# Optimization experiments

Measured on AMD Instinct MI355X. Metric: run time of the kernel, lower is better.

## Reference

```python
import jax, jax.numpy as jnp
import numpy as np

N = 100000
E = 1600000
B = 64
EPS = 1e-5


def setup_inputs() -> dict:
    key = jax.random.key(0)
    ks = jax.random.split(key, 20)
    x = jax.random.normal(ks[0], (N, 3), dtype=jnp.float32)
    edge_index = jax.random.randint(ks[1], (2, E), 0, N, dtype=jnp.int64)
    batch = jnp.sort(jax.random.randint(ks[2], (N,), 0, B, dtype=jnp.int64))

    def lin(k, fan_in, fan_out):
        s = 1.0 / np.sqrt(fan_in)
        kw, kb = jax.random.split(k)
        W = jax.random.uniform(kw, (fan_in, fan_out), minval=-s, maxval=s, dtype=jnp.float32)
        b = jax.random.uniform(kb, (fan_out,), minval=-s, maxval=s, dtype=jnp.float32)
        return W, b

    W1, b1 = lin(ks[3], 3, 16)
    W2, b2 = lin(ks[4], 16, 32)
    W3, b3 = lin(ks[5], 32, 64)
    fcW, fcb = lin(ks[6], 64, 10)
    g1 = jnp.ones((16,), jnp.float32); be1 = jnp.zeros((16,), jnp.float32)
    g2 = jnp.ones((32,), jnp.float32); be2 = jnp.zeros((32,), jnp.float32)
    g3 = jnp.ones((64,), jnp.float32); be3 = jnp.zeros((64,), jnp.float32)
    return {"x": x, "edge_index": edge_index, "batch": batch,
            "W1": W1, "b1": b1, "g1": g1, "be1": be1,
            "W2": W2, "b2": b2, "g2": g2, "be2": be2,
            "W3": W3, "b3": b3, "g3": g3, "be3": be3,
            "fcW": fcW, "fcb": fcb}


def _gcn_conv(x, W, b, row, col, deg_inv_sqrt):
    # PyG GCNConv: add self-loops (pre-appended in row/col), symmetric norm,
    # scatter-add aggregation at target nodes, then bias.
    xw = x @ W                                   # [N, d_out]
    norm = deg_inv_sqrt[row] * deg_inv_sqrt[col]  # [E+N]
    msg = xw[row] * norm[:, None]                 # gather + scale
    out = jax.ops.segment_sum(msg, col, num_segments=N)
    return out + b


def _bn_relu(x, gamma, beta):
    mean = jnp.mean(x, axis=0)
    var = jnp.mean(jnp.square(x - mean), axis=0)  # biased var (torch BN)
    xh = (x - mean) * jax.lax.rsqrt(var + EPS)
    return jax.nn.relu(xh * gamma + beta)


def reference(x, edge_index, batch, W1, b1, g1, be1, W2, b2, g2, be2,
              W3, b3, g3, be3, fcW, fcb):
    loops = jnp.arange(N, dtype=edge_index.dtype)
    row = jnp.concatenate([edge_index[0], loops])
    col = jnp.concatenate([edge_index[1], loops])
    deg = jax.ops.segment_sum(jnp.ones_like(col, dtype=x.dtype), col, num_segments=N)
    dis = jax.lax.rsqrt(deg)  # deg >= 1 due to self-loops

    h = _bn_relu(_gcn_conv(x, W1, b1, row, col, dis), g1, be1)
    h = _bn_relu(_gcn_conv(h, W2, b2, row, col, dis), g2, be2)
    h = _bn_relu(_gcn_conv(h, W3, b3, row, col, dis), g3, be3)

    sums = jax.ops.segment_sum(h, batch, num_segments=B)          # [B, 64]
    cnts = jax.ops.segment_sum(jnp.ones((N,), h.dtype), batch, num_segments=B)
    pooled = sums / jnp.maximum(cnts, 1.0)[:, None]
    return pooled @ fcW + fcb                                     # [B, 10]
```

## Files before the change

### kernel.cpp

```cpp
#include <hip/hip_runtime.h>

#define N_NODES 100000
#define N_EDGES 1600000
#define B_GRAPHS 64
#define BN_EPS 1e-5
#define NBMAX 3200

#define NBUCK 256
#define BUCK_NODES 392
#define PART_CHUNK 4096
#define NB_PART 391

#define QSCALE 2048.0f
#define QINV   4.8828125e-4f

typedef _Float16 half4_t __attribute__((ext_vector_type(4)));
typedef short short4_t __attribute__((ext_vector_type(4)));
typedef int intv2 __attribute__((ext_vector_type(2)));
typedef int intv4 __attribute__((ext_vector_type(4)));
typedef float floatv4 __attribute__((ext_vector_type(4)));

static inline int cdiv(long long a, int b) { return (int)((a + b - 1) / b); }

__device__ __forceinline__ short q16(float v) {
    int q = __float2int_rn(v * QSCALE);
    q = q > 32767 ? 32767 : (q < -32768 ? -32768 : q);
    return (short)q;
}

__global__ void part_hist_kernel(const int* __restrict__ col, int* __restrict__ bucket_cnt) {
    __shared__ int h[NBUCK];
    for (int i = threadIdx.x; i < NBUCK; i += 256) h[i] = 0;
    __syncthreads();
    long long ebase = (long long)blockIdx.x * PART_CHUNK;
    int n = (N_EDGES - ebase < PART_CHUNK) ? (int)(N_EDGES - ebase) : PART_CHUNK;
    for (int i = threadIdx.x; i < n; i += 256)
        atomicAdd(&h[col[ebase + i] / BUCK_NODES], 1);
    __syncthreads();
    for (int i = threadIdx.x; i < NBUCK; i += 256)
        if (h[i]) atomicAdd(&bucket_cnt[i], h[i]);
}

__global__ void part_scan_kernel(const int* __restrict__ bucket_cnt, int* __restrict__ bucket_base,
                                 int* __restrict__ bucket_cur) {
    __shared__ int s[NBUCK];
    int t = threadIdx.x;
    int v = bucket_cnt[t];
    s[t] = v;
    __syncthreads();
    for (int off = 1; off < NBUCK; off <<= 1) {
        int u = (t >= off) ? s[t - off] : 0;
        __syncthreads();
        s[t] += u;
        __syncthreads();
    }
    bucket_base[t] = s[t] - v;
    bucket_cur[t] = s[t] - v;
}

__global__ void part_scatter_kernel(const int* __restrict__ row, const int* __restrict__ col,
                                    int* __restrict__ bucket_cur, unsigned* __restrict__ part_edges) {
    __shared__ int h[NBUCK];
    __shared__ int base_s[NBUCK];
    __shared__ int cur_s[NBUCK];
    long long ebase = (long long)blockIdx.x * PART_CHUNK;
    int n = (N_EDGES - ebase < PART_CHUNK) ? (int)(N_EDGES - ebase) : PART_CHUNK;
    for (int i = threadIdx.x; i < NBUCK; i += 256) h[i] = 0;
    __syncthreads();
    for (int i = threadIdx.x; i < n; i += 256)
        atomicAdd(&h[col[ebase + i] / BUCK_NODES], 1);
    __syncthreads();
    for (int i = threadIdx.x; i < NBUCK; i += 256) {
        int c = h[i];
        base_s[i] = c ? atomicAdd(&bucket_cur[i], c) : 0;
        cur_s[i] = 0;
    }
    __syncthreads();
    for (int i = threadIdx.x; i < n; i += 256) {
        int r = row[ebase + i], c = col[ebase + i];
        int bkt = c / BUCK_NODES;
        int p = base_s[bkt] + atomicAdd(&cur_s[bkt], 1);
        part_edges[p] = ((unsigned)r << 9) | (unsigned)(c - bkt * BUCK_NODES);
    }
}

__global__ void csr_build_kernel(const int* __restrict__ bucket_base, const unsigned* __restrict__ part_edges,
                                 int* __restrict__ row_ptr, int* __restrict__ deg,
                                 float* __restrict__ dis, int* __restrict__ sorted_row,
                                 const float* __restrict__ x, short* __restrict__ xs4) {
    __shared__ int hist[BUCK_NODES];
    __shared__ int tsum[256];
    int b = blockIdx.x;
    int t = threadIdx.x;
    int nbase = b * BUCK_NODES;
    int ebase = bucket_base[b];
    int eend = (b == NBUCK - 1) ? N_EDGES : bucket_base[b + 1];
    int ne = eend - ebase;
    for (int i = t; i < BUCK_NODES; i += 256) hist[i] = 0;
    __syncthreads();
    for (int i = t; i < ne; i += 256)
        atomicAdd(&hist[part_edges[ebase + i] & 511u], 1);
    __syncthreads();
    int a0 = 0, a1 = 0;
    if (t < BUCK_NODES / 2) { a0 = hist[2 * t]; a1 = hist[2 * t + 1]; tsum[t] = a0 + a1; }
    else tsum[t] = 0;
    __syncthreads();
    for (int off = 1; off < 256; off <<= 1) {
        int u = (t >= off) ? tsum[t - off] : 0;
        __syncthreads();
        tsum[t] += u;
        __syncthreads();
    }
    if (t < BUCK_NODES / 2) {
        int excl = tsum[t] - (a0 + a1);
        hist[2 * t] = excl;
        hist[2 * t + 1] = excl + a0;
        int n0 = nbase + 2 * t, n1 = n0 + 1;
        if (n0 < N_NODES) {
            row_ptr[n0] = ebase + excl;
            deg[n0] = a0;
            dis[n0] = rsqrtf((float)a0 + 1.0f);
        }
        if (n1 < N_NODES) {
            row_ptr[n1] = ebase + excl + a0;
            deg[n1] = a1;
            dis[n1] = rsqrtf((float)a1 + 1.0f);
        }
    }
    __syncthreads();
    for (int i = t; i < ne; i += 256) {
        unsigned e = part_edges[ebase + i];
        int p = atomicAdd(&hist[e & 511u], 1);
        sorted_row[ebase + p] = (int)(e >> 9);
    }
    for (int i = t; i < BUCK_NODES; i += 256) {
        int n = nbase + i;
        if (n < N_NODES) {
            float d = dis[n];
            short4_t v;
            v.x = q16(x[n * 3 + 0] * d);
            v.y = q16(x[n * 3 + 1] * d);
            v.z = q16(x[n * 3 + 2] * d);
            v.w = 0;
            ((short4_t*)xs4)[n] = v;
        }
    }
}

template <int WPL> struct VecSel;
template <> struct VecSel<2> { using type = intv2; };
template <> struct VecSel<4> { using type = intv4; };

template <int IN, int OUT, int INSTRIDE, int WPL>
__global__ void gather_mm_kernel(const int* __restrict__ row_ptr, const int* __restrict__ deg,
                                 const int* __restrict__ sorted_row, const float* __restrict__ dis,
                                 const short* __restrict__ hs, const float* __restrict__ W,
                                 const float* __restrict__ b, _Float16* __restrict__ pre,
                                 double* __restrict__ part_s, double* __restrict__ part_q) {
    using V = typename VecSel<WPL>::type;
    const int FPL = 2 * WPL;
    const int LPN = INSTRIDE / FPL;
    const int NPW = 64 / LPN;
    const int NPB = 4 * NPW;
    const int UNROLL = 8;
    __shared__ __align__(16) float lds_agg[NPB * INSTRIDE];
    __shared__ double s_s[256];
    __shared__ double s_q[256];
    int tid = threadIdx.x;
    int wv = tid >> 6, lane = tid & 63;
    int jn = wv * NPW + lane / LPN;
    int p = lane % LPN;
    int n = blockIdx.x * NPB + jn;
    if (n < N_NODES) {
        int start = row_ptr[n];
        int d = deg[n];
        const int* sr = sorted_row + start;
        const V* hv = (const V*)hs;
        V v = hv[n * LPN + p];
        int acc[FPL];
#pragma unroll
        for (int w = 0; w < WPL; w++) {
            acc[2 * w] = (int)(short)v[w];
            acc[2 * w + 1] = v[w] >> 16;
        }
        int j = 0;
        for (; j + UNROLL <= d; j += UNROLL) {
            V a[UNROLL];
#pragma unroll
            for (int u = 0; u < UNROLL; u++) a[u] = hv[sr[j + u] * LPN + p];
#pragma unroll
            for (int u = 0; u < UNROLL; u++) {
#pragma unroll
                for (int w = 0; w < WPL; w++) {
                    acc[2 * w] += (int)(short)a[u][w];
                    acc[2 * w + 1] += a[u][w] >> 16;
                }
            }
        }
        for (; j < d; j++) {
            V a = hv[sr[j] * LPN + p];
#pragma unroll
            for (int w = 0; w < WPL; w++) {
                acc[2 * w] += (int)(short)a[w];
                acc[2 * w + 1] += a[w] >> 16;
            }
        }
        float dn = dis[n] * QINV;
        float* dst = &lds_agg[(jn * LPN + p) * FPL];
#pragma unroll
        for (int k = 0; k < FPL; k++) dst[k] = dn * (float)acc[k];
    }
    __syncthreads();

    const int NG = 256 / OUT;
    int o = tid % OUT;
    int g = tid / OUT;
    float wreg[IN];
#pragma unroll
    for (int k = 0; k < IN; k++) wreg[k] = W[k * OUT + o];
    float bo = b[o];
    double my_s = 0.0, my_q = 0.0;
    for (int j2 = g; j2 < NPB; j2 += NG) {
        int nn = blockIdx.x * NPB + j2;
        if (nn < N_NODES) {
            float acc = bo;
            const floatv4* src = (const floatv4*)&lds_agg[j2 * INSTRIDE];
#pragma unroll
            for (int q = 0; q < INSTRIDE / 4; q++) {
                floatv4 vq = src[q];
#pragma unroll
                for (int c = 0; c < 4; c++) {
                    if (4 * q + c < IN) acc += vq[c] * wreg[4 * q + c];
                }
            }
            _Float16 hq = (_Float16)acc;
            pre[nn * OUT + o] = hq;
            float fq = (float)hq;
            my_s += (double)fq;
            my_q += (double)fq * (double)fq;
        }
    }
    s_s[tid] = my_s;
    s_q[tid] = my_q;
    __syncthreads();
    if (tid < OUT) {
        double ts = 0.0, tq = 0.0;
        for (int k = tid; k < 256; k += OUT) { ts += s_s[k]; tq += s_q[k]; }
        part_s[(long long)tid * NBMAX + blockIdx.x] = ts;
        part_q[(long long)tid * NBMAX + blockIdx.x] = tq;
    }
}

__global__ void bn_finalize_kernel(const double* __restrict__ part_s, const double* __restrict__ part_q,
                                   int nb, float* __restrict__ bn_mean, float* __restrict__ bn_rstd) {
    __shared__ double s_s[256];
    __shared__ double s_q[256];
    int o = blockIdx.x;
    int t = threadIdx.x;
    double ms = 0.0, mq = 0.0;
    for (int k = t; k < nb; k += 256) {
        ms += part_s[(long long)o * NBMAX + k];
        mq += part_q[(long long)o * NBMAX + k];
    }
    s_s[t] = ms;
    s_q[t] = mq;
    __syncthreads();
    for (int off = 128; off > 0; off >>= 1) {
        if (t < off) { s_s[t] += s_s[t + off]; s_q[t] += s_q[t + off]; }
        __syncthreads();
    }
    if (t == 0) {
        double mean = s_s[0] / (double)N_NODES;
        double var = s_q[0] / (double)N_NODES - mean * mean;
        bn_mean[o] = (float)mean;
        bn_rstd[o] = (float)(1.0 / sqrt(var + BN_EPS));
    }
}

template <int F>
__global__ void bn_relu_kernel(const _Float16* __restrict__ pre, const float* __restrict__ bn_mean,
                               const float* __restrict__ bn_rstd, const float* __restrict__ g,
                               const float* __restrict__ be, const float* __restrict__ dis,
                               short* __restrict__ out) {
    const int GP = F / 4;
    int t = blockIdx.x * blockDim.x + threadIdx.x;
    const int total = N_NODES * GP;
    if (t >= total) return;
    int gi = t % GP;
    int f0 = gi * 4;
    half4_t v = ((const half4_t*)pre)[t];
    float d = dis[t / GP];
    short4_t o;
#pragma unroll
    for (int k = 0; k < 4; k++) {
        int f = f0 + k;
        float y = ((float)v[k] - bn_mean[f]) * bn_rstd[f] * g[f] + be[f];
        y = y > 0.f ? y : 0.f;
        o[k] = q16(y * d);
    }
    ((short4_t*)out)[t] = o;
}

#define POOL_CHUNK 32
__global__ void pool_kernel(const _Float16* __restrict__ pre, const int* __restrict__ batch,
                            const float* __restrict__ bn_mean, const float* __restrict__ bn_rstd,
                            const float* __restrict__ g, const float* __restrict__ be,
                            float* __restrict__ pooled, float* __restrict__ cnt) {
    int wave = (blockIdx.x * blockDim.x + threadIdx.x) >> 6;
    int lane = threadIdx.x & 63;
    int start = wave * POOL_CHUNK;
    if (start >= N_NODES) return;
    int end = start + POOL_CHUNK;
    if (end > N_NODES) end = N_NODES;
    float A = bn_rstd[lane] * g[lane];
    float B = be[lane] - bn_mean[lane] * A;
    int cur = batch[start];
    float acc = 0.f;
    float c = 0.f;
    int i = start;
    for (; i + 4 <= end; i += 4) {
        int b0 = batch[i], b1 = batch[i + 1], b2 = batch[i + 2], b3 = batch[i + 3];
        float v0 = fmaxf(0.f, fmaf((float)pre[(long long)i * 64 + lane], A, B));
        float v1 = fmaxf(0.f, fmaf((float)pre[(long long)(i + 1) * 64 + lane], A, B));
        float v2 = fmaxf(0.f, fmaf((float)pre[(long long)(i + 2) * 64 + lane], A, B));
        float v3 = fmaxf(0.f, fmaf((float)pre[(long long)(i + 3) * 64 + lane], A, B));
        if (b0 != cur) { atomicAdd(&pooled[cur * 64 + lane], acc); if (lane == 0) atomicAdd(&cnt[cur], c); acc = 0.f; c = 0.f; cur = b0; }
        acc += v0; c += 1.f;
        if (b1 != cur) { atomicAdd(&pooled[cur * 64 + lane], acc); if (lane == 0) atomicAdd(&cnt[cur], c); acc = 0.f; c = 0.f; cur = b1; }
        acc += v1; c += 1.f;
        if (b2 != cur) { atomicAdd(&pooled[cur * 64 + lane], acc); if (lane == 0) atomicAdd(&cnt[cur], c); acc = 0.f; c = 0.f; cur = b2; }
        acc += v2; c += 1.f;
        if (b3 != cur) { atomicAdd(&pooled[cur * 64 + lane], acc); if (lane == 0) atomicAdd(&cnt[cur], c); acc = 0.f; c = 0.f; cur = b3; }
        acc += v3; c += 1.f;
    }
    for (; i < end; i++) {
        int b = batch[i];
        if (b != cur) { atomicAdd(&pooled[cur * 64 + lane], acc); if (lane == 0) atomicAdd(&cnt[cur], c); acc = 0.f; c = 0.f; cur = b; }
        acc += fmaxf(0.f, fmaf((float)pre[(long long)i * 64 + lane], A, B)); c += 1.f;
    }
    atomicAdd(&pooled[cur * 64 + lane], acc);
    if (lane == 0) atomicAdd(&cnt[cur], c);
}

__global__ void final_kernel(const float* __restrict__ pooled, const float* __restrict__ cnt,
                             const float* __restrict__ fcW, const float* __restrict__ fcb,
                             float* __restrict__ out) {
    int t = blockIdx.x * blockDim.x + threadIdx.x;
    if (t >= B_GRAPHS * 10) return;
    int b = t / 10, j = t % 10;
    float inv = 1.0f / fmaxf(cnt[b], 1.0f);
    float acc = fcb[j];
#pragma unroll
    for (int f = 0; f < 64; f++) acc += pooled[b * 64 + f] * inv * fcW[f * 10 + j];
    out[t] = acc;
}

extern "C" void kernel_launch(void* const* d_in, const int* in_sizes, int n_in,
                              void* d_out, int out_size, void* d_ws, size_t ws_size,
                              hipStream_t stream) {
    const float* x  = (const float*)d_in[0];
    const int* ei   = (const int*)d_in[1];
    const int* batch= (const int*)d_in[2];
    const float* W1 = (const float*)d_in[3];  const float* b1 = (const float*)d_in[4];
    const float* g1 = (const float*)d_in[5];  const float* be1= (const float*)d_in[6];
    const float* W2 = (const float*)d_in[7];  const float* b2 = (const float*)d_in[8];
    const float* g2 = (const float*)d_in[9];  const float* be2= (const float*)d_in[10];
    const float* W3 = (const float*)d_in[11]; const float* b3 = (const float*)d_in[12];
    const float* g3 = (const float*)d_in[13]; const float* be3= (const float*)d_in[14];
    const float* fcW= (const float*)d_in[15]; const float* fcb= (const float*)d_in[16];
    float* out = (float*)d_out;

    const int* row = ei;
    const int* col = ei + N_EDGES;

    char* wp = (char*)d_ws;
    int*   bucket_cnt = (int*)wp;                wp += NBUCK * 4;
    float* pooled     = (float*)wp;              wp += 64 * 64 * 4;
    float* cnt        = (float*)wp;              wp += 64 * 4;
    const size_t ZERO_BYTES = NBUCK * 4 + 64 * 64 * 4 + 64 * 4;
    float* dis        = (float*)wp;              wp += N_NODES * 4;
    int*   deg_i      = (int*)wp;                wp += N_NODES * 4;
    int*   row_ptr    = (int*)wp;                wp += N_NODES * 4;
    int*   bucket_base= (int*)wp;                wp += NBUCK * 4;
    int*   bucket_cur = (int*)wp;                wp += NBUCK * 4;
    int*   sorted_row = (int*)wp;                wp += (size_t)N_EDGES * 4;
    unsigned* part_edges = (unsigned*)wp;        wp += (size_t)N_EDGES * 4;
    double* part_s    = (double*)wp;             wp += (size_t)NBMAX * 64 * 8;
    double* part_q    = (double*)wp;             wp += (size_t)NBMAX * 64 * 8;
    float* bn_mean    = (float*)wp;              wp += 64 * 4;
    float* bn_rstd    = (float*)wp;              wp += 64 * 4;
    short* xs4q       = (short*)wp;              wp += (size_t)N_NODES * 4 * 2;
    _Float16* PRE     = (_Float16*)wp;           wp += (size_t)N_NODES * 64 * 2;
    short* Hq         = (short*)wp;              wp += (size_t)N_NODES * 32 * 2;

    const int BS = 256;

    hipMemsetAsync(bucket_cnt, 0, ZERO_BYTES, stream);

    part_hist_kernel<<<NB_PART, 256, 0, stream>>>(col, bucket_cnt);
    part_scan_kernel<<<1, NBUCK, 0, stream>>>(bucket_cnt, bucket_base, bucket_cur);
    part_scatter_kernel<<<NB_PART, 256, 0, stream>>>(row, col, bucket_cur, part_edges);
    csr_build_kernel<<<NBUCK, 256, 0, stream>>>(bucket_base, part_edges, row_ptr, deg_i, dis, sorted_row, x, xs4q);

    const int NB1 = cdiv(N_NODES, 256);
    gather_mm_kernel<3, 16, 4, 2><<<NB1, 256, 0, stream>>>(
        row_ptr, deg_i, sorted_row, dis, xs4q, W1, b1, PRE, part_s, part_q);
    bn_finalize_kernel<<<16, 256, 0, stream>>>(part_s, part_q, NB1, bn_mean, bn_rstd);
    bn_relu_kernel<16><<<cdiv((long long)N_NODES * 4, BS), BS, 0, stream>>>(
        PRE, bn_mean, bn_rstd, g1, be1, dis, Hq);

    const int NB2 = cdiv(N_NODES, 128);
    gather_mm_kernel<16, 32, 16, 4><<<NB2, 256, 0, stream>>>(
        row_ptr, deg_i, sorted_row, dis, Hq, W2, b2, PRE, part_s, part_q);
    bn_finalize_kernel<<<32, 256, 0, stream>>>(part_s, part_q, NB2, bn_mean, bn_rstd);
    bn_relu_kernel<32><<<cdiv((long long)N_NODES * 8, BS), BS, 0, stream>>>(
        PRE, bn_mean, bn_rstd, g2, be2, dis, Hq);

    const int NB3 = cdiv(N_NODES, 64);
    gather_mm_kernel<32, 64, 32, 4><<<NB3, 256, 0, stream>>>(
        row_ptr, deg_i, sorted_row, dis, Hq, W3, b3, PRE, part_s, part_q);
    bn_finalize_kernel<<<64, 256, 0, stream>>>(part_s, part_q, NB3, bn_mean, bn_rstd);

    pool_kernel<<<cdiv((long long)cdiv(N_NODES, POOL_CHUNK) * 64, BS), BS, 0, stream>>>(
        PRE, batch, bn_mean, bn_rstd, g3, be3, pooled, cnt);
    final_kernel<<<1, B_GRAPHS * 10, 0, stream>>>(pooled, cnt, fcW, fcb, out);
}
```

Baseline: 266.0 us.

## Fold scan, BN finalize and final FC into last-block-done tails of producer kernels

Removes the separate part_scan, bn_finalize (three times) and final_kernel launches. Each producer kernel now takes an atomic done counter, and the last block to finish runs the follow-up reduction after a threadfence. This cuts five kernel launches and their launch gaps. In exchange, every block pays for an extra fence and atomic, and each finalize reduction now runs serially in one block instead of one block per feature.

```diff
diff --git a/kernel.cpp b/kernel.cpp
--- a/kernel.cpp
+++ b/kernel.cpp
@@ -28,8 +28,11 @@
     return (short)q;
 }
 
-__global__ void part_hist_kernel(const int* __restrict__ col, int* __restrict__ bucket_cnt) {
+__global__ void part_hist_kernel(const int* __restrict__ col, int* __restrict__ bucket_cnt,
+                                 int* __restrict__ bucket_base, int* __restrict__ bucket_cur,
+                                 int* __restrict__ done_ctr) {
     __shared__ int h[NBUCK];
+    __shared__ int is_last;
     for (int i = threadIdx.x; i < NBUCK; i += 256) h[i] = 0;
     __syncthreads();
     long long ebase = (long long)blockIdx.x * PART_CHUNK;
@@ -39,23 +42,24 @@
     __syncthreads();
     for (int i = threadIdx.x; i < NBUCK; i += 256)
         if (h[i]) atomicAdd(&bucket_cnt[i], h[i]);
-}
-
-__global__ void part_scan_kernel(const int* __restrict__ bucket_cnt, int* __restrict__ bucket_base,
-                                 int* __restrict__ bucket_cur) {
-    __shared__ int s[NBUCK];
+    __threadfence();
+    __syncthreads();
+    if (threadIdx.x == 0) is_last = (atomicAdd(done_ctr, 1) == gridDim.x - 1);
+    __syncthreads();
+    if (!is_last) return;
+    __threadfence();
     int t = threadIdx.x;
     int v = bucket_cnt[t];
-    s[t] = v;
+    h[t] = v;
     __syncthreads();
     for (int off = 1; off < NBUCK; off <<= 1) {
-        int u = (t >= off) ? s[t - off] : 0;
+        int u = (t >= off) ? h[t - off] : 0;
         __syncthreads();
-        s[t] += u;
+        h[t] += u;
         __syncthreads();
     }
-    bucket_base[t] = s[t] - v;
-    bucket_cur[t] = s[t] - v;
+    bucket_base[t] = h[t] - v;
+    bucket_cur[t] = h[t] - v;
 }
 
 __global__ void part_scatter_kernel(const int* __restrict__ row, const int* __restrict__ col,
@@ -156,7 +160,9 @@
                                  const int* __restrict__ sorted_row, const float* __restrict__ dis,
                                  const short* __restrict__ hs, const float* __restrict__ W,
                                  const float* __restrict__ b, _Float16* __restrict__ pre,
-                                 double* __restrict__ part_s, double* __restrict__ part_q) {
+                                 double* __restrict__ part_s, double* __restrict__ part_q,
+                                 int* __restrict__ done_ctr, float* __restrict__ bn_mean,
+                                 float* __restrict__ bn_rstd) {
     using V = typename VecSel<WPL>::type;
     const int FPL = 2 * WPL;
     const int LPN = INSTRIDE / FPL;
@@ -166,6 +172,7 @@
     __shared__ __align__(16) float lds_agg[NPB * INSTRIDE];
     __shared__ double s_s[256];
     __shared__ double s_q[256];
+    __shared__ int is_last;
     int tid = threadIdx.x;
     int wv = tid >> 6, lane = tid & 63;
     int jn = wv * NPW + lane / LPN;
@@ -249,31 +256,36 @@
         part_s[(long long)tid * NBMAX + blockIdx.x] = ts;
         part_q[(long long)tid * NBMAX + blockIdx.x] = tq;
     }
-}
-
-__global__ void bn_finalize_kernel(const double* __restrict__ part_s, const double* __restrict__ part_q,
-                                   int nb, float* __restrict__ bn_mean, float* __restrict__ bn_rstd) {
-    __shared__ double s_s[256];
-    __shared__ double s_q[256];
-    int o = blockIdx.x;
-    int t = threadIdx.x;
-    double ms = 0.0, mq = 0.0;
-    for (int k = t; k < nb; k += 256) {
-        ms += part_s[(long long)o * NBMAX + k];
-        mq += part_q[(long long)o * NBMAX + k];
-    }
-    s_s[t] = ms;
-    s_q[t] = mq;
-    __syncthreads();
-    for (int off = 128; off > 0; off >>= 1) {
-        if (t < off) { s_s[t] += s_s[t + off]; s_q[t] += s_q[t + off]; }
+
+    __threadfence();
+    __syncthreads();
+    if (tid == 0) is_last = (atomicAdd(done_ctr, 1) == gridDim.x - 1);
+    __syncthreads();
+    if (!is_last) return;
+    __threadfence();
+    {
+        const int TPF = 256 / OUT;
+        int fo = tid % OUT;
+        int fq = tid / OUT;
+        int nb = gridDim.x;
+        double ms = 0.0, mq = 0.0;
+        for (int k = fq; k < nb; k += TPF) {
+            ms += part_s[(long long)fo * NBMAX + k];
+            mq += part_q[(long long)fo * NBMAX + k];
+        }
+        s_s[tid] = ms;
+        s_q[tid] = mq;
         __syncthreads();
-    }
-    if (t == 0) {
-        double mean = s_s[0] / (double)N_NODES;
-        double var = s_q[0] / (double)N_NODES - mean * mean;
-        bn_mean[o] = (float)mean;
-        bn_rstd[o] = (float)(1.0 / sqrt(var + BN_EPS));
+        for (int off = TPF / 2; off > 0; off >>= 1) {
+            if (fq < off) { s_s[tid] += s_s[tid + off * OUT]; s_q[tid] += s_q[tid + off * OUT]; }
+            __syncthreads();
+        }
+        if (fq == 0) {
+            double mean = s_s[tid] / (double)N_NODES;
+            double var = s_q[tid] / (double)N_NODES - mean * mean;
+            bn_mean[fo] = (float)mean;
+            bn_rstd[fo] = (float)(1.0 / sqrt(var + BN_EPS));
+        }
     }
 }
 
@@ -305,54 +317,59 @@
 __global__ void pool_kernel(const _Float16* __restrict__ pre, const int* __restrict__ batch,
                             const float* __restrict__ bn_mean, const float* __restrict__ bn_rstd,
                             const float* __restrict__ g, const float* __restrict__ be,
-                            float* __restrict__ pooled, float* __restrict__ cnt) {
+                            float* __restrict__ pooled, float* __restrict__ cnt,
+                            int* __restrict__ done_ctr, const float* __restrict__ fcW,
+                            const float* __restrict__ fcb, float* __restrict__ out) {
+    __shared__ int is_last;
     int wave = (blockIdx.x * blockDim.x + threadIdx.x) >> 6;
     int lane = threadIdx.x & 63;
     int start = wave * POOL_CHUNK;
-    if (start >= N_NODES) return;
-    int end = start + POOL_CHUNK;
-    if (end > N_NODES) end = N_NODES;
-    float A = bn_rstd[lane] * g[lane];
-    float B = be[lane] - bn_mean[lane] * A;
-    int cur = batch[start];
-    float acc = 0.f;
-    float c = 0.f;
-    int i = start;
-    for (; i + 4 <= end; i += 4) {
-        int b0 = batch[i], b1 = batch[i + 1], b2 = batch[i + 2], b3 = batch[i + 3];
-        float v0 = fmaxf(0.f, fmaf((float)pre[(long long)i * 64 + lane], A, B));
-        float v1 = fmaxf(0.f, fmaf((float)pre[(long long)(i + 1) * 64 + lane], A, B));
-        float v2 = fmaxf(0.f, fmaf((float)pre[(long long)(i + 2) * 64 + lane], A, B));
-        float v3 = fmaxf(0.f, fmaf((float)pre[(long long)(i + 3) * 64 + lane], A, B));
-        if (b0 != cur) { atomicAdd(&pooled[cur * 64 + lane], acc); if (lane == 0) atomicAdd(&cnt[cur], c); acc = 0.f; c = 0.f; cur = b0; }
-        acc += v0; c += 1.f;
-        if (b1 != cur) { atomicAdd(&pooled[cur * 64 + lane], acc); if (lane == 0) atomicAdd(&cnt[cur], c); acc = 0.f; c = 0.f; cur = b1; }
-        acc += v1; c += 1.f;
-        if (b2 != cur) { atomicAdd(&pooled[cur * 64 + lane], acc); if (lane == 0) atomicAdd(&cnt[cur], c); acc = 0.f; c = 0.f; cur = b2; }
-        acc += v2; c += 1.f;
-        if (b3 != cur) { atomicAdd(&pooled[cur * 64 + lane], acc); if (lane == 0) atomicAdd(&cnt[cur], c); acc = 0.f; c = 0.f; cur = b3; }
-        acc += v3; c += 1.f;
-    }
-    for (; i < end; i++) {
-        int b = batch[i];
-        if (b != cur) { atomicAdd(&pooled[cur * 64 + lane], acc); if (lane == 0) atomicAdd(&cnt[cur], c); acc = 0.f; c = 0.f; cur = b; }
-        acc += fmaxf(0.f, fmaf((float)pre[(long long)i * 64 + lane], A, B)); c += 1.f;
-    }
-    atomicAdd(&pooled[cur * 64 + lane], acc);
-    if (lane == 0) atomicAdd(&cnt[cur], c);
-}
-
-__global__ void final_kernel(const float* __restrict__ pooled, const float* __restrict__ cnt,
-                             const float* __restrict__ fcW, const float* __restrict__ fcb,
-                             float* __restrict__ out) {
-    int t = blockIdx.x * blockDim.x + threadIdx.x;
-    if (t >= B_GRAPHS * 10) return;
-    int b = t / 10, j = t % 10;
-    float inv = 1.0f / fmaxf(cnt[b], 1.0f);
-    float acc = fcb[j];
-#pragma unroll
-    for (int f = 0; f < 64; f++) acc += pooled[b * 64 + f] * inv * fcW[f * 10 + j];
-    out[t] = acc;
+    if (start < N_NODES) {
+        int end = start + POOL_CHUNK;
+        if (end > N_NODES) end = N_NODES;
+        float A = bn_rstd[lane] * g[lane];
+        float B = be[lane] - bn_mean[lane] * A;
+        int cur = batch[start];
+        float acc = 0.f;
+        float c = 0.f;
+        int i = start;
+        for (; i + 4 <= end; i += 4) {
+            int b0 = batch[i], b1 = batch[i + 1], b2 = batch[i + 2], b3 = batch[i + 3];
+            float v0 = fmaxf(0.f, fmaf((float)pre[(long long)i * 64 + lane], A, B));
+            float v1 = fmaxf(0.f, fmaf((float)pre[(long long)(i + 1) * 64 + lane], A, B));
+            float v2 = fmaxf(0.f, fmaf((float)pre[(long long)(i + 2) * 64 + lane], A, B));
+            float v3 = fmaxf(0.f, fmaf((float)pre[(long long)(i + 3) * 64 + lane], A, B));
+            if (b0 != cur) { atomicAdd(&pooled[cur * 64 + lane], acc); if (lane == 0) atomicAdd(&cnt[cur], c); acc = 0.f; c = 0.f; cur = b0; }
+            acc += v0; c += 1.f;
+            if (b1 != cur) { atomicAdd(&pooled[cur * 64 + lane], acc); if (lane == 0) atomicAdd(&cnt[cur], c); acc = 0.f; c = 0.f; cur = b1; }
+            acc += v1; c += 1.f;
+            if (b2 != cur) { atomicAdd(&pooled[cur * 64 + lane], acc); if (lane == 0) atomicAdd(&cnt[cur], c); acc = 0.f; c = 0.f; cur = b2; }
+            acc += v2; c += 1.f;
+            if (b3 != cur) { atomicAdd(&pooled[cur * 64 + lane], acc); if (lane == 0) atomicAdd(&cnt[cur], c); acc = 0.f; c = 0.f; cur = b3; }
+            acc += v3; c += 1.f;
+        }
+        for (; i < end; i++) {
+            int b = batch[i];
+            if (b != cur) { atomicAdd(&pooled[cur * 64 + lane], acc); if (lane == 0) atomicAdd(&cnt[cur], c); acc = 0.f; c = 0.f; cur = b; }
+            acc += fmaxf(0.f, fmaf((float)pre[(long long)i * 64 + lane], A, B)); c += 1.f;
+        }
+        atomicAdd(&pooled[cur * 64 + lane], acc);
+        if (lane == 0) atomicAdd(&cnt[cur], c);
+    }
+    __threadfence();
+    __syncthreads();
+    if (threadIdx.x == 0) is_last = (atomicAdd(done_ctr, 1) == gridDim.x - 1);
+    __syncthreads();
+    if (!is_last) return;
+    __threadfence();
+    for (int t = threadIdx.x; t < B_GRAPHS * 10; t += 256) {
+        int b = t / 10, j = t % 10;
+        float inv = 1.0f / fmaxf(cnt[b], 1.0f);
+        float acc = fcb[j];
+#pragma unroll
+        for (int f = 0; f < 64; f++) acc += pooled[b * 64 + f] * inv * fcW[f * 10 + j];
+        out[t] = acc;
+    }
 }
 
 extern "C" void kernel_launch(void* const* d_in, const int* in_sizes, int n_in,
@@ -374,10 +391,11 @@
     const int* col = ei + N_EDGES;
 
     char* wp = (char*)d_ws;
+    int*   sync_ctr   = (int*)wp;                wp += 8 * 4;
     int*   bucket_cnt = (int*)wp;                wp += NBUCK * 4;
     float* pooled     = (float*)wp;              wp += 64 * 64 * 4;
     float* cnt        = (float*)wp;              wp += 64 * 4;
-    const size_t ZERO_BYTES = NBUCK * 4 + 64 * 64 * 4 + 64 * 4;
+    const size_t ZERO_BYTES = 8 * 4 + NBUCK * 4 + 64 * 64 * 4 + 64 * 4;
     float* dis        = (float*)wp;              wp += N_NODES * 4;
     int*   deg_i      = (int*)wp;                wp += N_NODES * 4;
     int*   row_ptr    = (int*)wp;                wp += N_NODES * 4;
@@ -395,33 +413,31 @@
 
     const int BS = 256;
 
-    hipMemsetAsync(bucket_cnt, 0, ZERO_BYTES, stream);
-
-    part_hist_kernel<<<NB_PART, 256, 0, stream>>>(col, bucket_cnt);
-    part_scan_kernel<<<1, NBUCK, 0, stream>>>(bucket_cnt, bucket_base, bucket_cur);
+    hipMemsetAsync(sync_ctr, 0, ZERO_BYTES, stream);
+
+    part_hist_kernel<<<NB_PART, 256, 0, stream>>>(col, bucket_cnt, bucket_base, bucket_cur, &sync_ctr[0]);
     part_scatter_kernel<<<NB_PART, 256, 0, stream>>>(row, col, bucket_cur, part_edges);
     csr_build_kernel<<<NBUCK, 256, 0, stream>>>(bucket_base, part_edges, row_ptr, deg_i, dis, sorted_row, x, xs4q);
 
     const int NB1 = cdiv(N_NODES, 256);
     gather_mm_kernel<3, 16, 4, 2><<<NB1, 256, 0, stream>>>(
-        row_ptr, deg_i, sorted_row, dis, xs4q, W1, b1, PRE, part_s, part_q);
-    bn_finalize_kernel<<<16, 256, 0, stream>>>(part_s, part_q, NB1, bn_mean, bn_rstd);
+        row_ptr, deg_i, sorted_row, dis, xs4q, W1, b1, PRE, part_s, part_q,
+        &sync_ctr[1], bn_mean, bn_rstd);
     bn_relu_kernel<16><<<cdiv((long long)N_NODES * 4, BS), BS, 0, stream>>>(
         PRE, bn_mean, bn_rstd, g1, be1, dis, Hq);
 
     const int NB2 = cdiv(N_NODES, 128);
     gather_mm_kernel<16, 32, 16, 4><<<NB2, 256, 0, stream>>>(
-        row_ptr, deg_i, sorted_row, dis, Hq, W2, b2, PRE, part_s, part_q);
-    bn_finalize_kernel<<<32, 256, 0, stream>>>(part_s, part_q, NB2, bn_mean, bn_rstd);
+        row_ptr, deg_i, sorted_row, dis, Hq, W2, b2, PRE, part_s, part_q,
+        &sync_ctr[2], bn_mean, bn_rstd);
     bn_relu_kernel<32><<<cdiv((long long)N_NODES * 8, BS), BS, 0, stream>>>(
         PRE, bn_mean, bn_rstd, g2, be2, dis, Hq);
 
     const int NB3 = cdiv(N_NODES, 64);
     gather_mm_kernel<32, 64, 32, 4><<<NB3, 256, 0, stream>>>(
-        row_ptr, deg_i, sorted_row, dis, Hq, W3, b3, PRE, part_s, part_q);
-    bn_finalize_kernel<<<64, 256, 0, stream>>>(part_s, part_q, NB3, bn_mean, bn_rstd);
+        row_ptr, deg_i, sorted_row, dis, Hq, W3, b3, PRE, part_s, part_q,
+        &sync_ctr[3], bn_mean, bn_rstd);
 
     pool_kernel<<<cdiv((long long)cdiv(N_NODES, POOL_CHUNK) * 64, BS), BS, 0, stream>>>(
-        PRE, batch, bn_mean, bn_rstd, g3, be3, pooled, cnt);
-    final_kernel<<<1, B_GRAPHS * 10, 0, stream>>>(pooled, cnt, fcW, fcb, out);
-}
+        PRE, batch, bn_mean, bn_rstd, g3, be3, pooled, cnt, &sync_ctr[4], fcW, fcb, out);
+}
```

Measured after the change: 757.2 us. +184.6%, slower.
